# Kernel optimization log

Measured on AMD Instinct MI355X. Metric: run time of the kernel, lower is better.

## Reference

```python
import jax, jax.numpy as jnp
import numpy as np

P_TOKENS = 200  # num_prompt_tokens
N_HEADS = 4


def setup_inputs() -> dict:
    key = jax.random.key(0)
    ks = jax.random.split(key, 6)
    B, N, C = 64, 1224, 1024
    D = 256  # bottleneck / down_size
    s = 0.02
    return {
        "x": jax.random.normal(ks[0], (B, N, C), dtype=jnp.float32),
        "down_W": jax.random.normal(ks[1], (D, C), dtype=jnp.float32) * s,
        "down_b": jnp.zeros((D,), jnp.float32),
        "up_W": jax.random.normal(ks[2], (C, D), dtype=jnp.float32) * s,
        "up_b": jnp.zeros((C,), jnp.float32),
        "in_proj_W": jax.random.normal(ks[3], (3 * D, D), dtype=jnp.float32) * s,
        "in_proj_b": jnp.zeros((3 * D,), jnp.float32),
        "out_proj_W": jax.random.normal(ks[4], (D, D), dtype=jnp.float32) * s,
        "out_proj_b": jnp.zeros((D,), jnp.float32),
        "gate": jnp.float32(1.0),
    }


def _forward(x, down_W, down_b, up_W, up_b, in_proj_W, in_proj_b,
             out_proj_W, out_proj_b, gate):
    B, N, C = x.shape
    E = down_W.shape[0]
    hd = E // N_HEADS
    # down projection + exact GELU (torch nn.GELU default)
    down = jax.nn.gelu(x @ down_W.T + down_b, approximate=False)  # [B,N,E]
    prompt = down[:, :P_TOKENS, :]   # [B,P,E]
    tok = down[:, P_TOKENS:, :]      # [B,T,E]
    # --- nn.MultiheadAttention(prompt, prompt, prompt) ---
    qkv = prompt @ in_proj_W.T + in_proj_b            # [B,P,3E]
    q, k, v = jnp.split(qkv, 3, axis=-1)
    def heads(t):
        return t.reshape(B, P_TOKENS, N_HEADS, hd)
    q, k, v = heads(q), heads(k), heads(v)
    attn = jnp.einsum('bqhd,bkhd->bhqk', q, k) / jnp.sqrt(jnp.float32(hd))
    attn = jax.nn.softmax(attn, axis=-1)
    sa = jnp.einsum('bhqk,bkhd->bqhd', attn, v).reshape(B, P_TOKENS, E)
    sa = sa @ out_proj_W.T + out_proj_b               # [B,P,E]
    # --- manual cross attention prompt -> tokens ---
    scale = jnp.float32(E) ** -0.5
    cross = jax.nn.softmax(jnp.einsum('bpe,bte->bpt', sa, tok) * scale, axis=-1)
    prompt_out = jnp.einsum('bpt,bte->bpe', cross, tok)  # [B,P,E]
    combined = jnp.concatenate([prompt_out, tok], axis=1)  # [B,N,E]
    up = combined @ up_W.T + up_b                          # [B,N,C]
    return gate * up


def reference(x, down_W, down_b, up_W, up_b, in_proj_W, in_proj_b,
              out_proj_W, out_proj_b, gate):
    return _forward(x, down_W, down_b, up_W, up_b, in_proj_W, in_proj_b,
                    out_proj_W, out_proj_b, gate)
```

## Files before the change

### kernel.cpp

```cpp
#include <hip/hip_runtime.h>
#include <math.h>

#define BB 64
#define NN 1224
#define CC 1024
#define DD 256
#define PP 200
#define TT 1024
#define HH 4
#define HDD 64

typedef __attribute__((ext_vector_type(8))) short bf16x8;
typedef __attribute__((ext_vector_type(4))) float f32x4;
typedef unsigned short u16;
typedef unsigned long long u64;

__device__ __forceinline__ u16 f2bf(float f) {
  union { float f; unsigned int u; } v; v.f = f;
  unsigned int r = v.u + 0x7FFF + ((v.u >> 16) & 1);
  return (u16)(r >> 16);
}
__device__ __forceinline__ float bf2f(u16 h) {
  union { unsigned int u; float f; } v; v.u = ((unsigned int)h) << 16;
  return v.f;
}
__device__ __forceinline__ unsigned int pk2(float a, float b) {
  return (unsigned int)f2bf(a) | ((unsigned int)f2bf(b) << 16);
}
__device__ __forceinline__ void gload16(const void* g, void* l) {
  __builtin_amdgcn_global_load_lds(
      (const __attribute__((address_space(1))) void*)g,
      (__attribute__((address_space(3))) void*)l, 16, 0, 0);
}
__device__ __forceinline__ f32x4 ntld4(const float* p) {
  return __builtin_nontemporal_load((const f32x4*)p);
}

static const size_t SZ_DOWN = (size_t)BB * NN * DD * 2;
static const size_t SZ_TOKT = (size_t)BB * DD * TT * 2;
static const size_t SZ_Q    = (size_t)BB * HH * PP * HDD * 2;
static const size_t SZ_SCORES = (size_t)BB * PP * TT * 2;

static const size_t B_DOWN   = 0;
static const size_t B_TOKT   = B_DOWN + SZ_DOWN;
static const size_t B_POOL   = B_TOKT + SZ_TOKT;
static const size_t B_QB     = B_POOL;
static const size_t B_KB     = B_QB + SZ_Q;
static const size_t B_VB     = B_KB + SZ_Q;
static const size_t B_SA     = B_VB + SZ_Q;
static const size_t B_SA2    = B_SA + SZ_Q;
static const size_t B_POUTBF = B_SA2;
static const size_t B_SCORES = B_SA2 + SZ_Q;
static const size_t B_PBF    = B_SCORES;
static const size_t B_W      = B_SCORES + SZ_SCORES * 2;
static const size_t B_WD     = B_W;
static const size_t B_WU     = B_WD + 524288;
static const size_t B_WIP    = B_WU + 524288;
static const size_t B_WOP    = B_WIP + 393216;

#define MFMA_STEP64(Ab, Bb) \
  _Pragma("unroll") \
  for (int kk = 0; kk < 64; kk += 32) { \
    bf16x8 af[4], bfr[2]; \
    _Pragma("unroll") \
    for (int mi = 0; mi < 4; ++mi) { \
      const int R = mi * 16 + (lane & 15); \
      const int byt = (R * 128 + (kk + (lane >> 4) * 8) * 2) ^ ((R & 7) << 4); \
      af[mi] = *(const bf16x8*)((const char*)Ab + byt); \
    } \
    _Pragma("unroll") \
    for (int ni = 0; ni < 2; ++ni) { \
      const int R = wave * 32 + ni * 16 + (lane & 15); \
      const int byt = (R * 128 + (kk + (lane >> 4) * 8) * 2) ^ ((R & 7) << 4); \
      bfr[ni] = *(const bf16x8*)((const char*)Bb + byt); \
    } \
    _Pragma("unroll") \
    for (int mi = 0; mi < 4; ++mi) \
      _Pragma("unroll") \
      for (int ni = 0; ni < 2; ++ni) \
        acc[mi][ni] = __builtin_amdgcn_mfma_f32_16x16x32_bf16(af[mi], bfr[ni], acc[mi][ni], 0, 0, 0); \
  }

#define MFMA_AF(SACC, K0, Bbuf) \
  _Pragma("unroll") \
  for (int kk = 0; kk < 64; kk += 32) { \
    bf16x8 af[4], bfr[2]; \
    _Pragma("unroll") \
    for (int mi = 0; mi < 4; ++mi) { \
      const int R = mi * 16 + (lane & 15); \
      const int byt = (R * 512 + ((K0) + kk + (lane >> 4) * 8) * 2) ^ ((R & 7) << 4); \
      af[mi] = *(const bf16x8*)((const char*)Afull + byt); \
    } \
    _Pragma("unroll") \
    for (int ni = 0; ni < 2; ++ni) { \
      const int R = wave * 32 + ni * 16 + (lane & 15); \
      const int byt = (R * 128 + (kk + (lane >> 4) * 8) * 2) ^ ((R & 7) << 4); \
      bfr[ni] = *(const bf16x8*)((const char*)Bbuf + byt); \
    } \
    _Pragma("unroll") \
    for (int mi = 0; mi < 4; ++mi) \
      _Pragma("unroll") \
      for (int ni = 0; ni < 2; ++ni) \
        SACC[mi][ni] = __builtin_amdgcn_mfma_f32_16x16x32_bf16(af[mi], bfr[ni], SACC[mi][ni], 0, 0, 0); \
  }

#define GLOAD_A1(Ab, SRC) \
  { \
    const int L = wave * 1024 + lane * 16; \
    const int r = L >> 7; \
    const int ce = ((L & 127) ^ ((r & 7) << 4)) >> 1; \
    gload16((SRC), (char*)Ab + wave * 1024); \
  }

#define GLOAD_B4(Bb, SRC) \
  _Pragma("unroll") \
  for (int ii = 0; ii < 4; ++ii) { \
    const int slot = wave * 4 + ii; \
    const int L = slot * 1024 + lane * 16; \
    const int r = L >> 7; \
    const int ce = ((L & 127) ^ ((r & 7) << 4)) >> 1; \
    gload16((SRC), (char*)Bb + slot * 1024); \
  }

#define PIPE_WAIT(N) asm volatile("s_waitcnt vmcnt(" #N ")" ::: "memory");
#define PIPE_BAR() \
  __builtin_amdgcn_s_barrier(); \
  __builtin_amdgcn_sched_barrier(0);
#define PIPE_END() \
  asm volatile("s_waitcnt lgkmcnt(0)" ::: "memory"); \
  __builtin_amdgcn_s_barrier(); \
  __builtin_amdgcn_sched_barrier(0);

__global__ __launch_bounds__(256) void k_castw(const float* __restrict__ dW,
                                               const float* __restrict__ uW,
                                               const float* __restrict__ iW,
                                               const float* __restrict__ oW,
                                               u16* __restrict__ dWb, u16* __restrict__ uWb,
                                               u16* __restrict__ iWb, u16* __restrict__ oWb)
{
  const int id = blockIdx.x * 256 + threadIdx.x;
  const float* s; u16* d; int off;
  if (id < 65536)       { s = dW; d = dWb; off = id; }
  else if (id < 131072) { s = uW; d = uWb; off = id - 65536; }
  else if (id < 180224) { s = iW; d = iWb; off = id - 131072; }
  else                  { s = oW; d = oWb; off = id - 180224; }
  const float4 v = ((const float4*)s)[off];
  uint2 p; p.x = pk2(v.x, v.y); p.y = pk2(v.z, v.w);
  *(uint2*)&d[(size_t)off * 4] = p;
}

__global__ __launch_bounds__(512) void k_down(const float* __restrict__ x,
                                              const u16* __restrict__ Wd,
                                              const float* __restrict__ bias,
                                              u16* __restrict__ out,
                                              u16* __restrict__ tokT)
{
  __shared__ u16 Ab[2][64 * 64];
  __shared__ u16 Bb[2][256 * 64];
  const int tid = threadIdx.x;
  const int lane = tid & 63, wave = tid >> 6;
  f32x4 acc[4][2] = {};
  const int m0 = blockIdx.x * 64;
  const int ar0 = tid >> 4;
  const int c4 = (tid & 15) * 4;

  f32x4 areg[2];
#pragma unroll
  for (int i = 0; i < 2; ++i)
    areg[i] = ntld4(&x[(size_t)(m0 + ar0 + 32 * i) * CC + c4]);
#pragma unroll
  for (int i = 0; i < 2; ++i) {
    const int r = ar0 + 32 * i;
    uint2 p; p.x = pk2(areg[i].x, areg[i].y); p.y = pk2(areg[i].z, areg[i].w);
    *(uint2*)((char*)Ab[0] + ((r * 128 + c4 * 2) ^ ((r & 7) << 4))) = p;
  }
  GLOAD_B4(Bb[0], &Wd[(size_t)r * CC + 0 + ce])
#pragma unroll
  for (int i = 0; i < 2; ++i)
    areg[i] = ntld4(&x[(size_t)(m0 + ar0 + 32 * i) * CC + 64 + c4]);

  for (int it = 0; it < 16; ++it) {
    const int cur = it & 1;
    if (it < 14) {
#pragma unroll
      for (int i = 0; i < 2; ++i) {
        const int r = ar0 + 32 * i;
        uint2 p; p.x = pk2(areg[i].x, areg[i].y); p.y = pk2(areg[i].z, areg[i].w);
        *(uint2*)((char*)Ab[cur ^ 1] + ((r * 128 + c4 * 2) ^ ((r & 7) << 4))) = p;
      }
      const int kx = (it + 2) * 64;
#pragma unroll
      for (int i = 0; i < 2; ++i)
        areg[i] = ntld4(&x[(size_t)(m0 + ar0 + 32 * i) * CC + kx + c4]);
      const int kb = (it + 1) * 64;
      GLOAD_B4(Bb[cur ^ 1], &Wd[(size_t)r * CC + kb + ce])
      asm volatile("s_waitcnt vmcnt(6) lgkmcnt(0)" ::: "memory");
    } else if (it == 14) {
#pragma unroll
      for (int i = 0; i < 2; ++i) {
        const int r = ar0 + 32 * i;
        uint2 p; p.x = pk2(areg[i].x, areg[i].y); p.y = pk2(areg[i].z, areg[i].w);
        *(uint2*)((char*)Ab[cur ^ 1] + ((r * 128 + c4 * 2) ^ ((r & 7) << 4))) = p;
      }
      GLOAD_B4(Bb[cur ^ 1], &Wd[(size_t)r * CC + 960 + ce])
      asm volatile("s_waitcnt vmcnt(4) lgkmcnt(0)" ::: "memory");
    } else {
      asm volatile("s_waitcnt vmcnt(0) lgkmcnt(0)" ::: "memory");
    }
    PIPE_BAR()
    MFMA_STEP64(Ab[cur], Bb[cur])
    PIPE_END()
  }
#pragma unroll
  for (int mi = 0; mi < 4; ++mi) {
#pragma unroll
    for (int ni = 0; ni < 2; ++ni) {
      const int col = wave * 32 + ni * 16 + (lane & 15);
      const float bv = bias[col];
      u16 vs[4];
#pragma unroll
      for (int r = 0; r < 4; ++r) {
        const int row = m0 + mi * 16 + (lane >> 4) * 4 + r;
        float v = acc[mi][ni][r] + bv;
        v = 0.5f * v * (1.f + erff(v * 0.7071067811865475f));
        vs[r] = f2bf(v);
        out[(size_t)row * DD + col] = vs[r];
      }
      const int row0 = m0 + mi * 16 + (lane >> 4) * 4;
      const int b = row0 / NN, rr = row0 - b * NN;
      if (rr >= PP) {
        const u64 pk = (u64)vs[0] | ((u64)vs[1] << 16) | ((u64)vs[2] << 32) | ((u64)vs[3] << 48);
        *(u64*)&tokT[((size_t)(b * DD + col)) * TT + (rr - PP)] = pk;
      }
    }
  }
}

__global__ __launch_bounds__(512) void k_qkv(const u16* __restrict__ down,
                                             const u16* __restrict__ Wip,
                                             const float* __restrict__ bias,
                                             u16* __restrict__ qb,
                                             u16* __restrict__ kb,
                                             u16* __restrict__ vb)
{
  __shared__ u16 Ab[2][64 * 64];
  __shared__ u16 Bb[2][256 * 64];
  const int tid = threadIdx.x;
  const int lane = tid & 63, wave = tid >> 6;
  f32x4 acc[4][2] = {};
  const int m0 = blockIdx.x * 64;
  const int nt = blockIdx.y;

#define QKV_A(BUF, K0) GLOAD_A1(BUF, ({ const int m = m0 + r; const int b = m / PP; const int p = m - b * PP; \
                    &down[((size_t)(b * NN + p)) * DD + (K0) + ce]; }))
  QKV_A(Ab[0], 0)
  GLOAD_B4(Bb[0], &Wip[(size_t)(nt * 256 + r) * DD + 0 + ce])
  for (int it = 0; it < 4; ++it) {
    const int cur = it & 1;
    if (it < 3) {
      const int k0 = (it + 1) * 64;
      QKV_A(Ab[cur ^ 1], k0)
      GLOAD_B4(Bb[cur ^ 1], &Wip[(size_t)(nt * 256 + r) * DD + k0 + ce])
      PIPE_WAIT(5)
    } else { PIPE_WAIT(0) }
    PIPE_BAR()
    MFMA_STEP64(Ab[cur], Bb[cur])
    PIPE_END()
  }
#undef QKV_A
  u16* dst = (nt == 0) ? qb : ((nt == 1) ? kb : vb);
#pragma unroll
  for (int mi = 0; mi < 4; ++mi) {
#pragma unroll
    for (int ni = 0; ni < 2; ++ni) {
      const int n = wave * 32 + ni * 16 + (lane & 15);
      const float bv = bias[nt * 256 + n];
      const int h = n >> 6, dd = n & 63;
#pragma unroll
      for (int r = 0; r < 4; ++r) {
        const int m = m0 + mi * 16 + (lane >> 4) * 4 + r;
        const int b = m / PP, p = m - b * PP;
        dst[(((size_t)(b * HH + h)) * PP + p) * HDD + dd] = f2bf(acc[mi][ni][r] + bv);
      }
    }
  }
}

__global__ __launch_bounds__(512) void k_attn(const u16* __restrict__ qb,
                                              const u16* __restrict__ kb,
                                              const u16* __restrict__ vb,
                                              u16* __restrict__ sa)
{
  __shared__ u16 Ks[208 * 64];
  __shared__ u16 Vt[64 * 232];
  __shared__ u16 Pb[8 * 16 * 232];
  const int tid = threadIdx.x, lane = tid & 63, wave = tid >> 6;
  const int bh = blockIdx.x;
  const size_t kvbase = (size_t)bh * (PP * HDD);

  for (int it = 0; it < 7; ++it) {
    const int idx = tid + 512 * it;
    if (idx < 3200) {
      const int e = idx * 4;
      const int j = e >> 6, d = e & 63;
      const u64 kv = *(const u64*)&kb[kvbase + e];
      const int byt = (j * 128 + d * 2) ^ ((j & 7) << 4);
      *(u64*)((char*)Ks + byt) = kv;
      const u64 vv = *(const u64*)&vb[kvbase + e];
      const u16* vp = (const u16*)&vv;
#pragma unroll
      for (int w = 0; w < 4; ++w) Vt[(d + w) * 232 + j] = vp[w];
    }
  }
  if (tid < 128) {
    const int rr = 200 + (tid >> 4), c = (tid & 15) * 4;
    const int byt = (rr * 128 + c * 2) ^ ((rr & 7) << 4);
    *(u64*)((char*)Ks + byt) = 0ULL;
  }
  {
    const int d = tid >> 3, cg = tid & 7;
    *(u64*)&Vt[d * 232 + 200 + cg * 4] = 0ULL;
  }
  {
    u16* pw = Pb + wave * (16 * 232);
#pragma unroll
    for (int w = 0; w < 2; ++w) {
      const int idx = lane + 64 * w;
      if (idx < 96) {
        const int row = idx / 6, cg = idx - row * 6;
        *(u64*)&pw[row * 232 + 208 + cg * 4] = 0ULL;
      }
    }
  }
  __syncthreads();

  const int b_ = bh >> 2, h = bh & 3;
  const u16* qbase = qb + kvbase;
  u16* pw = Pb + wave * (16 * 232);

  for (int f = wave; f < 13; f += 8) {
    int qrow = f * 16 + (lane & 15); if (qrow > 199) qrow = 199;
    bf16x8 qa[2];
#pragma unroll
    for (int kk = 0; kk < 2; ++kk)
      qa[kk] = *(const bf16x8*)&qbase[(size_t)qrow * 64 + kk * 32 + (lane >> 4) * 8];

    f32x4 s[13];
#pragma unroll
    for (int nf = 0; nf < 13; ++nf) {
      const int R = nf * 16 + (lane & 15);
      f32x4 a = {};
#pragma unroll
      for (int kk = 0; kk < 2; ++kk) {
        const int byt = (R * 128 + (kk * 32 + (lane >> 4) * 8) * 2) ^ ((R & 7) << 4);
        const bf16x8 kf = *(const bf16x8*)((const char*)Ks + byt);
        a = __builtin_amdgcn_mfma_f32_16x16x32_bf16(qa[kk], kf, a, 0, 0, 0);
      }
      s[nf] = a;
    }
    float mx[4] = {-1e30f, -1e30f, -1e30f, -1e30f};
#pragma unroll
    for (int nf = 0; nf < 13; ++nf) {
      const int col = nf * 16 + (lane & 15);
#pragma unroll
      for (int r = 0; r < 4; ++r) {
        float v = (col < PP) ? s[nf][r] * 0.125f : -INFINITY;
        s[nf][r] = v;
        mx[r] = fmaxf(mx[r], v);
      }
    }
#pragma unroll
    for (int off = 1; off < 16; off <<= 1)
#pragma unroll
      for (int r = 0; r < 4; ++r) mx[r] = fmaxf(mx[r], __shfl_xor(mx[r], off));
    float sum[4] = {0.f, 0.f, 0.f, 0.f};
#pragma unroll
    for (int nf = 0; nf < 13; ++nf)
#pragma unroll
      for (int r = 0; r < 4; ++r) {
        const float e = expf(s[nf][r] - mx[r]);
        s[nf][r] = e;
        sum[r] += e;
      }
#pragma unroll
    for (int off = 1; off < 16; off <<= 1)
#pragma unroll
      for (int r = 0; r < 4; ++r) sum[r] += __shfl_xor(sum[r], off);
    float inv[4];
#pragma unroll
    for (int r = 0; r < 4; ++r) inv[r] = 1.f / sum[r];
#pragma unroll
    for (int nf = 0; nf < 13; ++nf) {
      const int col = nf * 16 + (lane & 15);
#pragma unroll
      for (int r = 0; r < 4; ++r) {
        const int row = (lane >> 4) * 4 + r;
        pw[row * 232 + col] = f2bf(s[nf][r] * inv[r]);
      }
    }
    f32x4 o[4] = {};
#pragma unroll
    for (int kk = 0; kk < 7; ++kk) {
      const bf16x8 pa = *(const bf16x8*)((const char*)pw +
                         ((lane & 15) * 232 + kk * 32 + (lane >> 4) * 8) * 2);
#pragma unroll
      for (int nf4 = 0; nf4 < 4; ++nf4) {
        const bf16x8 vv = *(const bf16x8*)((const char*)Vt +
                           (((lane & 15) + 16 * nf4) * 232 + kk * 32 + (lane >> 4) * 8) * 2);
        o[nf4] = __builtin_amdgcn_mfma_f32_16x16x32_bf16(pa, vv, o[nf4], 0, 0, 0);
      }
    }
#pragma unroll
    for (int nf4 = 0; nf4 < 4; ++nf4) {
      const int d = (lane & 15) + 16 * nf4;
#pragma unroll
      for (int r = 0; r < 4; ++r) {
        const int p = f * 16 + (lane >> 4) * 4 + r;
        if (p < PP)
          sa[((size_t)(b_ * PP + p)) * DD + h * HDD + d] = f2bf(o[nf4][r]);
      }
    }
  }
}

__global__ __launch_bounds__(512, 2) void k_fuse(const u16* __restrict__ A,
                                                 const u16* __restrict__ Wop,
                                                 const float* __restrict__ bias,
                                                 const u16* __restrict__ down,
                                                 u16* __restrict__ pbf)
{
  __shared__ u16 Ab[2][64 * 64];
  __shared__ u16 Bb[2][256 * 64];
  __shared__ u16 Afull[64 * 256];
  __shared__ float Mred[8][64];
  __shared__ float Lred[8][64];
  const int tid = threadIdx.x;
  const int lane = tid & 63, wave = tid >> 6;
  const int b = blockIdx.x, mh = blockIdx.y;
  const int m0 = mh * 64;

  f32x4 acc[4][2] = {};
#define FU_A(BUF, K0) GLOAD_A1(BUF, ({ int p = m0 + r; p = (p < PP) ? p : (PP - 1); \
                    &A[((size_t)(b * PP + p)) * DD + (K0) + ce]; }))
  FU_A(Ab[0], 0)
  GLOAD_B4(Bb[0], &Wop[(size_t)r * DD + 0 + ce])
  for (int it = 0; it < 4; ++it) {
    const int cur = it & 1;
    if (it < 3) {
      const int k0 = (it + 1) * 64;
      FU_A(Ab[cur ^ 1], k0)
      GLOAD_B4(Bb[cur ^ 1], &Wop[(size_t)r * DD + k0 + ce])
      PIPE_WAIT(5)
    } else { PIPE_WAIT(0) }
    PIPE_BAR()
    MFMA_STEP64(Ab[cur], Bb[cur])
    PIPE_END()
  }
#undef FU_A

  GLOAD_B4(Bb[0], &down[((size_t)(b * NN + PP + r)) * DD + 0 + ce])

#pragma unroll
  for (int mi = 0; mi < 4; ++mi) {
#pragma unroll
    for (int ni = 0; ni < 2; ++ni) {
      const int col = wave * 32 + ni * 16 + (lane & 15);
      const float bv = bias[col];
#pragma unroll
      for (int r = 0; r < 4; ++r) {
        const int row = mi * 16 + (lane >> 4) * 4 + r;
        *(u16*)((char*)Afull + ((row * 512 + col * 2) ^ ((row & 7) << 4))) =
            f2bf(acc[mi][ni][r] + bv);
      }
    }
  }
  __syncthreads();

  f32x4 s4[4][4][2] = {};
#pragma unroll
  for (int st = 0; st < 16; ++st) {
    const int cur = st & 1;
    if (st < 15) {
      const int nx = st + 1;
      const int nt2 = nx >> 2, k02 = (nx & 3) * 64;
      GLOAD_B4(Bb[cur ^ 1], &down[((size_t)(b * NN + PP + nt2 * 256 + r)) * DD + k02 + ce])
      PIPE_WAIT(4)
    } else { PIPE_WAIT(0) }
    PIPE_BAR()
    {
      const int k0s = (st & 3) * 64;
      MFMA_AF(s4[st >> 2], k0s, Bb[cur])
    }
    PIPE_END()
  }

  float mx[4][4];
#pragma unroll
  for (int mi = 0; mi < 4; ++mi)
#pragma unroll
    for (int r = 0; r < 4; ++r) mx[mi][r] = -1e30f;
#pragma unroll
  for (int nt = 0; nt < 4; ++nt)
#pragma unroll
    for (int mi = 0; mi < 4; ++mi)
#pragma unroll
      for (int ni = 0; ni < 2; ++ni)
#pragma unroll
        for (int r = 0; r < 4; ++r) {
          const float v = s4[nt][mi][ni][r] * 0.0625f;
          s4[nt][mi][ni][r] = v;
          mx[mi][r] = fmaxf(mx[mi][r], v);
        }
#pragma unroll
  for (int off = 1; off < 16; off <<= 1)
#pragma unroll
    for (int mi = 0; mi < 4; ++mi)
#pragma unroll
      for (int r = 0; r < 4; ++r) mx[mi][r] = fmaxf(mx[mi][r], __shfl_xor(mx[mi][r], off));
  if ((lane & 15) == 0) {
#pragma unroll
    for (int mi = 0; mi < 4; ++mi)
#pragma unroll
      for (int r = 0; r < 4; ++r)
        Mred[wave][mi * 16 + (lane >> 4) * 4 + r] = mx[mi][r];
  }
  __syncthreads();
  float M[4][4];
#pragma unroll
  for (int mi = 0; mi < 4; ++mi)
#pragma unroll
    for (int r = 0; r < 4; ++r) {
      const int row = mi * 16 + (lane >> 4) * 4 + r;
      float m = Mred[0][row];
#pragma unroll
      for (int w = 1; w < 8; ++w) m = fmaxf(m, Mred[w][row]);
      M[mi][r] = m;
    }
  float l[4][4];
#pragma unroll
  for (int mi = 0; mi < 4; ++mi)
#pragma unroll
    for (int r = 0; r < 4; ++r) l[mi][r] = 0.f;
#pragma unroll
  for (int nt = 0; nt < 4; ++nt)
#pragma unroll
    for (int mi = 0; mi < 4; ++mi)
#pragma unroll
      for (int ni = 0; ni < 2; ++ni)
#pragma unroll
        for (int r = 0; r < 4; ++r) {
          const float e = __expf(s4[nt][mi][ni][r] - M[mi][r]);
          s4[nt][mi][ni][r] = e;
          l[mi][r] += e;
        }
#pragma unroll
  for (int off = 1; off < 16; off <<= 1)
#pragma unroll
    for (int mi = 0; mi < 4; ++mi)
#pragma unroll
      for (int r = 0; r < 4; ++r) l[mi][r] += __shfl_xor(l[mi][r], off);
  if ((lane & 15) == 0) {
#pragma unroll
    for (int mi = 0; mi < 4; ++mi)
#pragma unroll
      for (int r = 0; r < 4; ++r)
        Lred[wave][mi * 16 + (lane >> 4) * 4 + r] = l[mi][r];
  }
  __syncthreads();
  float inv[4][4];
#pragma unroll
  for (int mi = 0; mi < 4; ++mi)
#pragma unroll
    for (int r = 0; r < 4; ++r) {
      const int row = mi * 16 + (lane >> 4) * 4 + r;
      float t = 0.f;
#pragma unroll
      for (int w = 0; w < 8; ++w) t += Lred[w][row];
      inv[mi][r] = 1.f / t;
    }

#pragma unroll
  for (int nt = 0; nt < 4; ++nt)
#pragma unroll
    for (int mi = 0; mi < 4; ++mi)
#pragma unroll
      for (int ni = 0; ni < 2; ++ni) {
        const int t = nt * 256 + wave * 32 + ni * 16 + (lane & 15);
#pragma unroll
        for (int r = 0; r < 4; ++r) {
          const int p = m0 + mi * 16 + (lane >> 4) * 4 + r;
          if (p < PP)
            pbf[((size_t)(b * PP + p)) * TT + t] = f2bf(s4[nt][mi][ni][r] * inv[mi][r]);
        }
      }
}

__global__ __launch_bounds__(512) void k_pout(const u16* __restrict__ pbf,
                                              const u16* __restrict__ tokT,
                                              u16* __restrict__ out)
{
  __shared__ u16 Ab[2][64 * 64];
  __shared__ u16 Bb[2][256 * 64];
  const int tid = threadIdx.x;
  const int lane = tid & 63, wave = tid >> 6;
  f32x4 acc[4][2] = {};
  const int b = blockIdx.x, mh = blockIdx.y;

#define PO_A(BUF, K0) GLOAD_A1(BUF, ({ int p = mh * 64 + r; p = (p < PP) ? p : (PP - 1); \
                    &pbf[((size_t)(b * PP + p)) * TT + (K0) + ce]; }))
  PO_A(Ab[0], 0)
  GLOAD_B4(Bb[0], &tokT[((size_t)(b * DD + r)) * TT + 0 + ce])
  for (int it = 0; it < 16; ++it) {
    const int cur = it & 1;
    if (it < 15) {
      const int k0 = (it + 1) * 64;
      PO_A(Ab[cur ^ 1], k0)
      GLOAD_B4(Bb[cur ^ 1], &tokT[((size_t)(b * DD + r)) * TT + k0 + ce])
      PIPE_WAIT(5)
    } else { PIPE_WAIT(0) }
    PIPE_BAR()
    MFMA_STEP64(Ab[cur], Bb[cur])
    PIPE_END()
  }
#undef PO_A
#pragma unroll
  for (int mi = 0; mi < 4; ++mi) {
#pragma unroll
    for (int ni = 0; ni < 2; ++ni) {
      const int e = wave * 32 + ni * 16 + (lane & 15);
#pragma unroll
      for (int r = 0; r < 4; ++r) {
        const int p = mh * 64 + mi * 16 + (lane >> 4) * 4 + r;
        if (p < PP)
          out[((size_t)(b * PP + p)) * DD + e] = f2bf(acc[mi][ni][r]);
      }
    }
  }
}

__global__ __launch_bounds__(512) void k_up(const u16* __restrict__ poutbf,
                                            const u16* __restrict__ down,
                                            const u16* __restrict__ Wu,
                                            const float* __restrict__ bias,
                                            const float* __restrict__ gate,
                                            float* __restrict__ out)
{
  __shared__ u16 Ab[2][64 * 64];
  __shared__ u16 Bb[2][256 * 64];
  const int tid = threadIdx.x;
  const int lane = tid & 63, wave = tid >> 6;
  f32x4 acc[4][2] = {};
  const int m0 = blockIdx.x * 64;
  const int n0 = blockIdx.y * 256;

#define UP_A(BUF, K0) GLOAD_A1(BUF, ({ const int m = m0 + r; const int b = m / NN; const int rr = m - b * NN; \
                     const u16* base = (rr < PP) ? &poutbf[((size_t)(b * PP + rr)) * DD] \
                                                 : &down[((size_t)(b * NN + rr)) * DD]; \
                     base + (K0) + ce; }))
  UP_A(Ab[0], 0)
  GLOAD_B4(Bb[0], &Wu[(size_t)(n0 + r) * DD + 0 + ce])
  for (int it = 0; it < 4; ++it) {
    const int cur = it & 1;
    if (it < 3) {
      const int k0 = (it + 1) * 64;
      UP_A(Ab[cur ^ 1], k0)
      GLOAD_B4(Bb[cur ^ 1], &Wu[(size_t)(n0 + r) * DD + k0 + ce])
      PIPE_WAIT(5)
    } else { PIPE_WAIT(0) }
    PIPE_BAR()
    MFMA_STEP64(Ab[cur], Bb[cur])
    PIPE_END()
  }
#undef UP_A
  const float g = gate[0];
#pragma unroll
  for (int mi = 0; mi < 4; ++mi) {
#pragma unroll
    for (int ni = 0; ni < 2; ++ni) {
      const int col = n0 + wave * 32 + ni * 16 + (lane & 15);
      const float bv = bias[col];
#pragma unroll
      for (int r = 0; r < 4; ++r) {
        const int row = m0 + mi * 16 + (lane >> 4) * 4 + r;
        __builtin_nontemporal_store((acc[mi][ni][r] + bv) * g, &out[(size_t)row * CC + col]);
      }
    }
  }
}

extern "C" void kernel_launch(void* const* d_in, const int* in_sizes, int n_in,
                              void* d_out, int out_size, void* d_ws, size_t ws_size,
                              hipStream_t stream) {
  const float* x          = (const float*)d_in[0];
  const float* down_W     = (const float*)d_in[1];
  const float* down_b     = (const float*)d_in[2];
  const float* up_W       = (const float*)d_in[3];
  const float* up_b       = (const float*)d_in[4];
  const float* in_proj_W  = (const float*)d_in[5];
  const float* in_proj_b  = (const float*)d_in[6];
  const float* out_proj_W = (const float*)d_in[7];
  const float* out_proj_b = (const float*)d_in[8];
  const float* gate       = (const float*)d_in[9];
  float* out = (float*)d_out;

  char* wsb = (char*)d_ws;
  u16* down_bf = (u16*)(wsb + B_DOWN);
  u16* tokT    = (u16*)(wsb + B_TOKT);
  u16* qb      = (u16*)(wsb + B_QB);
  u16* kb      = (u16*)(wsb + B_KB);
  u16* vb      = (u16*)(wsb + B_VB);
  u16* sa_bf   = (u16*)(wsb + B_SA);
  u16* pbf     = (u16*)(wsb + B_PBF);
  u16* poutbf  = (u16*)(wsb + B_POUTBF);
  u16* Wd  = (u16*)(wsb + B_WD);
  u16* Wu  = (u16*)(wsb + B_WU);
  u16* Wip = (u16*)(wsb + B_WIP);
  u16* Wop = (u16*)(wsb + B_WOP);

  k_castw<<<dim3(768), 256, 0, stream>>>(down_W, up_W, in_proj_W, out_proj_W, Wd, Wu, Wip, Wop);
  k_down<<<dim3((BB * NN) / 64), 512, 0, stream>>>(x, Wd, down_b, down_bf, tokT);
  k_qkv<<<dim3(200, 3), 512, 0, stream>>>(down_bf, Wip, in_proj_b, qb, kb, vb);
  k_attn<<<dim3(BB * HH), 512, 0, stream>>>(qb, kb, vb, sa_bf);
  k_fuse<<<dim3(BB, 4), 512, 0, stream>>>(sa_bf, Wop, out_proj_b, down_bf, pbf);
  k_pout<<<dim3(BB, 4), 512, 0, stream>>>(pbf, tokT, poutbf);
  k_up<<<dim3((BB * NN) / 64, CC / 256), 512, 0, stream>>>(poutbf, down_bf, Wu, up_b, gate, out);
}
```

Measured before the change: 306.0 us.

## Fuse cross-attention P·V into k_fuse, dropping the pbf round trip

The cross-attention probability matrix no longer goes to global memory for a separate k_pout kernel. It is written unnormalized to shared memory in two halves and multiplied against tokT inside k_fuse, with the softmax normalization applied at the end. This removes a kernel launch and the write and read of a 64x200x1024 bf16 buffer. In exchange, shared memory grows to a 128KB pool, occupancy drops to one block per CU, and the per-block serial work gets longer with only 256 blocks.

```diff
diff --git a/kernel.cpp b/kernel.cpp
--- a/kernel.cpp
+++ b/kernel.cpp
@@ -51,7 +51,6 @@
 static const size_t B_SA2    = B_SA + SZ_Q;
 static const size_t B_POUTBF = B_SA2;
 static const size_t B_SCORES = B_SA2 + SZ_Q;
-static const size_t B_PBF    = B_SCORES;
 static const size_t B_W      = B_SCORES + SZ_SCORES * 2;
 static const size_t B_WD     = B_W;
 static const size_t B_WU     = B_WD + 524288;
@@ -66,13 +65,13 @@
     for (int mi = 0; mi < 4; ++mi) { \
       const int R = mi * 16 + (lane & 15); \
       const int byt = (R * 128 + (kk + (lane >> 4) * 8) * 2) ^ ((R & 7) << 4); \
-      af[mi] = *(const bf16x8*)((const char*)Ab + byt); \
+      af[mi] = *(const bf16x8*)((const char*)(Ab) + byt); \
     } \
     _Pragma("unroll") \
     for (int ni = 0; ni < 2; ++ni) { \
       const int R = wave * 32 + ni * 16 + (lane & 15); \
       const int byt = (R * 128 + (kk + (lane >> 4) * 8) * 2) ^ ((R & 7) << 4); \
-      bfr[ni] = *(const bf16x8*)((const char*)Bb + byt); \
+      bfr[ni] = *(const bf16x8*)((const char*)(Bb) + byt); \
     } \
     _Pragma("unroll") \
     for (int mi = 0; mi < 4; ++mi) \
@@ -95,13 +94,36 @@
     for (int ni = 0; ni < 2; ++ni) { \
       const int R = wave * 32 + ni * 16 + (lane & 15); \
       const int byt = (R * 128 + (kk + (lane >> 4) * 8) * 2) ^ ((R & 7) << 4); \
-      bfr[ni] = *(const bf16x8*)((const char*)Bbuf + byt); \
+      bfr[ni] = *(const bf16x8*)((const char*)(Bbuf) + byt); \
     } \
     _Pragma("unroll") \
     for (int mi = 0; mi < 4; ++mi) \
       _Pragma("unroll") \
       for (int ni = 0; ni < 2; ++ni) \
         SACC[mi][ni] = __builtin_amdgcn_mfma_f32_16x16x32_bf16(af[mi], bfr[ni], SACC[mi][ni], 0, 0, 0); \
+  }
+
+#define MFMA_PV(O, T0, Bbuf) \
+  _Pragma("unroll") \
+  for (int kk = 0; kk < 64; kk += 32) { \
+    bf16x8 af[4], bfr[2]; \
+    _Pragma("unroll") \
+    for (int mi = 0; mi < 4; ++mi) { \
+      const int R = mi * 16 + (lane & 15); \
+      const int byt = (R * 1024 + ((T0) + kk + (lane >> 4) * 8) * 2) ^ ((R & 7) << 4); \
+      af[mi] = *(const bf16x8*)((const char*)Ph + byt); \
+    } \
+    _Pragma("unroll") \
+    for (int ni = 0; ni < 2; ++ni) { \
+      const int R = wave * 32 + ni * 16 + (lane & 15); \
+      const int byt = (R * 128 + (kk + (lane >> 4) * 8) * 2) ^ ((R & 7) << 4); \
+      bfr[ni] = *(const bf16x8*)((const char*)(Bbuf) + byt); \
+    } \
+    _Pragma("unroll") \
+    for (int mi = 0; mi < 4; ++mi) \
+      _Pragma("unroll") \
+      for (int ni = 0; ni < 2; ++ni) \
+        O[mi][ni] = __builtin_amdgcn_mfma_f32_16x16x32_bf16(af[mi], bfr[ni], O[mi][ni], 0, 0, 0); \
   }
 
 #define GLOAD_A1(Ab, SRC) \
@@ -109,7 +131,7 @@
     const int L = wave * 1024 + lane * 16; \
     const int r = L >> 7; \
     const int ce = ((L & 127) ^ ((r & 7) << 4)) >> 1; \
-    gload16((SRC), (char*)Ab + wave * 1024); \
+    gload16((SRC), (char*)(Ab) + wave * 1024); \
   }
 
 #define GLOAD_B4(Bb, SRC) \
@@ -119,7 +141,7 @@
     const int L = slot * 1024 + lane * 16; \
     const int r = L >> 7; \
     const int ce = ((L & 127) ^ ((r & 7) << 4)) >> 1; \
-    gload16((SRC), (char*)Bb + slot * 1024); \
+    gload16((SRC), (char*)(Bb) + slot * 1024); \
   }
 
 #define PIPE_WAIT(N) asm volatile("s_waitcnt vmcnt(" #N ")" ::: "memory");
@@ -127,6 +149,10 @@
   __builtin_amdgcn_s_barrier(); \
   __builtin_amdgcn_sched_barrier(0);
 #define PIPE_END() \
+  asm volatile("s_waitcnt lgkmcnt(0)" ::: "memory"); \
+  __builtin_amdgcn_s_barrier(); \
+  __builtin_amdgcn_sched_barrier(0);
+#define LGKM_BAR() \
   asm volatile("s_waitcnt lgkmcnt(0)" ::: "memory"); \
   __builtin_amdgcn_s_barrier(); \
   __builtin_amdgcn_sched_barrier(0);
@@ -423,17 +449,22 @@
   }
 }
 
-__global__ __launch_bounds__(512, 2) void k_fuse(const u16* __restrict__ A,
+__global__ __launch_bounds__(512, 1) void k_fuse(const u16* __restrict__ A,
                                                  const u16* __restrict__ Wop,
                                                  const float* __restrict__ bias,
                                                  const u16* __restrict__ down,
-                                                 u16* __restrict__ pbf)
+                                                 const u16* __restrict__ tokT,
+                                                 u16* __restrict__ pout)
 {
-  __shared__ u16 Ab[2][64 * 64];
-  __shared__ u16 Bb[2][256 * 64];
-  __shared__ u16 Afull[64 * 256];
+  __shared__ __align__(16) char pool[131072];
   __shared__ float Mred[8][64];
   __shared__ float Lred[8][64];
+  u16* Bb0 = (u16*)pool;
+  u16* Bb1 = (u16*)(pool + 32768);
+  u16* Ab0 = (u16*)(pool + 65536);
+  u16* Ab1 = (u16*)(pool + 65536 + 8192);
+  u16* Afull = (u16*)(pool + 65536);
+  u16* Ph = (u16*)(pool + 65536);
   const int tid = threadIdx.x;
   const int lane = tid & 63, wave = tid >> 6;
   const int b = blockIdx.x, mh = blockIdx.y;
@@ -442,23 +473,26 @@
   f32x4 acc[4][2] = {};
 #define FU_A(BUF, K0) GLOAD_A1(BUF, ({ int p = m0 + r; p = (p < PP) ? p : (PP - 1); \
                     &A[((size_t)(b * PP + p)) * DD + (K0) + ce]; }))
-  FU_A(Ab[0], 0)
-  GLOAD_B4(Bb[0], &Wop[(size_t)r * DD + 0 + ce])
+  FU_A(Ab0, 0)
+  GLOAD_B4(Bb0, &Wop[(size_t)r * DD + 0 + ce])
   for (int it = 0; it < 4; ++it) {
-    const int cur = it & 1;
+    u16* Abc = (it & 1) ? Ab1 : Ab0;
+    u16* Bbc = (it & 1) ? Bb1 : Bb0;
+    u16* Abn = (it & 1) ? Ab0 : Ab1;
+    u16* Bbn = (it & 1) ? Bb0 : Bb1;
     if (it < 3) {
       const int k0 = (it + 1) * 64;
-      FU_A(Ab[cur ^ 1], k0)
-      GLOAD_B4(Bb[cur ^ 1], &Wop[(size_t)r * DD + k0 + ce])
+      FU_A(Abn, k0)
+      GLOAD_B4(Bbn, &Wop[(size_t)r * DD + k0 + ce])
       PIPE_WAIT(5)
     } else { PIPE_WAIT(0) }
     PIPE_BAR()
-    MFMA_STEP64(Ab[cur], Bb[cur])
+    MFMA_STEP64(Abc, Bbc)
     PIPE_END()
   }
 #undef FU_A
 
-  GLOAD_B4(Bb[0], &down[((size_t)(b * NN + PP + r)) * DD + 0 + ce])
+  GLOAD_B4(Bb0, &down[((size_t)(b * NN + PP + r)) * DD + 0 + ce])
 
 #pragma unroll
   for (int mi = 0; mi < 4; ++mi) {
@@ -474,25 +508,28 @@
       }
     }
   }
-  __syncthreads();
+  LGKM_BAR()
 
   f32x4 s4[4][4][2] = {};
 #pragma unroll
   for (int st = 0; st < 16; ++st) {
-    const int cur = st & 1;
+    u16* Bbc = (st & 1) ? Bb1 : Bb0;
+    u16* Bbn = (st & 1) ? Bb0 : Bb1;
     if (st < 15) {
       const int nx = st + 1;
       const int nt2 = nx >> 2, k02 = (nx & 3) * 64;
-      GLOAD_B4(Bb[cur ^ 1], &down[((size_t)(b * NN + PP + nt2 * 256 + r)) * DD + k02 + ce])
+      GLOAD_B4(Bbn, &down[((size_t)(b * NN + PP + nt2 * 256 + r)) * DD + k02 + ce])
       PIPE_WAIT(4)
     } else { PIPE_WAIT(0) }
     PIPE_BAR()
     {
       const int k0s = (st & 3) * 64;
-      MFMA_AF(s4[st >> 2], k0s, Bb[cur])
+      MFMA_AF(s4[st >> 2], k0s, Bbc)
     }
     PIPE_END()
   }
+
+  GLOAD_B4(Bb0, &tokT[((size_t)(b * DD + r)) * TT + 0 + ce])
 
   float mx[4][4];
 #pragma unroll
@@ -524,7 +561,7 @@
       for (int r = 0; r < 4; ++r)
         Mred[wave][mi * 16 + (lane >> 4) * 4 + r] = mx[mi][r];
   }
-  __syncthreads();
+  LGKM_BAR()
   float M[4][4];
 #pragma unroll
   for (int mi = 0; mi < 4; ++mi)
@@ -566,7 +603,7 @@
       for (int r = 0; r < 4; ++r)
         Lred[wave][mi * 16 + (lane >> 4) * 4 + r] = l[mi][r];
   }
-  __syncthreads();
+  LGKM_BAR()
   float inv[4][4];
 #pragma unroll
   for (int mi = 0; mi < 4; ++mi)
@@ -579,50 +616,56 @@
       inv[mi][r] = 1.f / t;
     }
 
-#pragma unroll
-  for (int nt = 0; nt < 4; ++nt)
-#pragma unroll
-    for (int mi = 0; mi < 4; ++mi)
-#pragma unroll
-      for (int ni = 0; ni < 2; ++ni) {
-        const int t = nt * 256 + wave * 32 + ni * 16 + (lane & 15);
-#pragma unroll
-        for (int r = 0; r < 4; ++r) {
-          const int p = m0 + mi * 16 + (lane >> 4) * 4 + r;
-          if (p < PP)
-            pbf[((size_t)(b * PP + p)) * TT + t] = f2bf(s4[nt][mi][ni][r] * inv[mi][r]);
-        }
-      }
-}
-
-__global__ __launch_bounds__(512) void k_pout(const u16* __restrict__ pbf,
-                                              const u16* __restrict__ tokT,
-                                              u16* __restrict__ out)
-{
-  __shared__ u16 Ab[2][64 * 64];
-  __shared__ u16 Bb[2][256 * 64];
-  const int tid = threadIdx.x;
-  const int lane = tid & 63, wave = tid >> 6;
-  f32x4 acc[4][2] = {};
-  const int b = blockIdx.x, mh = blockIdx.y;
-
-#define PO_A(BUF, K0) GLOAD_A1(BUF, ({ int p = mh * 64 + r; p = (p < PP) ? p : (PP - 1); \
-                    &pbf[((size_t)(b * PP + p)) * TT + (K0) + ce]; }))
-  PO_A(Ab[0], 0)
-  GLOAD_B4(Bb[0], &tokT[((size_t)(b * DD + r)) * TT + 0 + ce])
-  for (int it = 0; it < 16; ++it) {
-    const int cur = it & 1;
-    if (it < 15) {
-      const int k0 = (it + 1) * 64;
-      PO_A(Ab[cur ^ 1], k0)
-      GLOAD_B4(Bb[cur ^ 1], &tokT[((size_t)(b * DD + r)) * TT + k0 + ce])
-      PIPE_WAIT(5)
+  f32x4 o[4][2] = {};
+#define WRITE_P(NT0) \
+  _Pragma("unroll") \
+  for (int q = 0; q < 2; ++q) \
+    _Pragma("unroll") \
+    for (int mi = 0; mi < 4; ++mi) \
+      _Pragma("unroll") \
+      for (int ni = 0; ni < 2; ++ni) { \
+        const int tl = q * 256 + wave * 32 + ni * 16 + (lane & 15); \
+        _Pragma("unroll") \
+        for (int r = 0; r < 4; ++r) { \
+          const int row = mi * 16 + (lane >> 4) * 4 + r; \
+          *(u16*)((char*)Ph + ((row * 1024 + tl * 2) ^ ((row & 7) << 4))) = \
+              f2bf(s4[(NT0) + q][mi][ni][r]); \
+        } \
+      }
+
+  WRITE_P(0)
+  LGKM_BAR()
+#pragma unroll
+  for (int st = 0; st < 8; ++st) {
+    u16* Bbc = (st & 1) ? Bb1 : Bb0;
+    u16* Bbn = (st & 1) ? Bb0 : Bb1;
+    if (st < 7) {
+      GLOAD_B4(Bbn, &tokT[((size_t)(b * DD + r)) * TT + (st + 1) * 64 + ce])
+      PIPE_WAIT(4)
+    } else {
+      GLOAD_B4(Bbn, &tokT[((size_t)(b * DD + r)) * TT + 512 + ce])
+      PIPE_WAIT(4)
+    }
+    PIPE_BAR()
+    MFMA_PV(o, st * 64, Bbc)
+    PIPE_END()
+  }
+  WRITE_P(2)
+  LGKM_BAR()
+#pragma unroll
+  for (int st = 0; st < 8; ++st) {
+    u16* Bbc = (st & 1) ? Bb1 : Bb0;
+    u16* Bbn = (st & 1) ? Bb0 : Bb1;
+    if (st < 7) {
+      GLOAD_B4(Bbn, &tokT[((size_t)(b * DD + r)) * TT + 512 + (st + 1) * 64 + ce])
+      PIPE_WAIT(4)
     } else { PIPE_WAIT(0) }
     PIPE_BAR()
-    MFMA_STEP64(Ab[cur], Bb[cur])
+    MFMA_PV(o, st * 64, Bbc)
     PIPE_END()
   }
-#undef PO_A
+#undef WRITE_P
+
 #pragma unroll
   for (int mi = 0; mi < 4; ++mi) {
 #pragma unroll
@@ -630,9 +673,9 @@
       const int e = wave * 32 + ni * 16 + (lane & 15);
 #pragma unroll
       for (int r = 0; r < 4; ++r) {
-        const int p = mh * 64 + mi * 16 + (lane >> 4) * 4 + r;
+        const int p = m0 + mi * 16 + (lane >> 4) * 4 + r;
         if (p < PP)
-          out[((size_t)(b * PP + p)) * DD + e] = f2bf(acc[mi][ni][r]);
+          pout[((size_t)(b * PP + p)) * DD + e] = f2bf(o[mi][ni][r] * inv[mi][r]);
       }
     }
   }
@@ -710,7 +753,6 @@
   u16* kb      = (u16*)(wsb + B_KB);
   u16* vb      = (u16*)(wsb + B_VB);
   u16* sa_bf   = (u16*)(wsb + B_SA);
-  u16* pbf     = (u16*)(wsb + B_PBF);
   u16* poutbf  = (u16*)(wsb + B_POUTBF);
   u16* Wd  = (u16*)(wsb + B_WD);
   u16* Wu  = (u16*)(wsb + B_WU);
@@ -721,7 +763,6 @@
   k_down<<<dim3((BB * NN) / 64), 512, 0, stream>>>(x, Wd, down_b, down_bf, tokT);
   k_qkv<<<dim3(200, 3), 512, 0, stream>>>(down_bf, Wip, in_proj_b, qb, kb, vb);
   k_attn<<<dim3(BB * HH), 512, 0, stream>>>(qb, kb, vb, sa_bf);
-  k_fuse<<<dim3(BB, 4), 512, 0, stream>>>(sa_bf, Wop, out_proj_b, down_bf, pbf);
-  k_pout<<<dim3(BB, 4), 512, 0, stream>>>(pbf, tokT, poutbf);
+  k_fuse<<<dim3(BB, 4), 512, 0, stream>>>(sa_bf, Wop, out_proj_b, down_bf, tokT, poutbf);
   k_up<<<dim3((BB * NN) / 64, CC / 256), 512, 0, stream>>>(poutbf, down_bf, Wu, up_b, gate, out);
 }
```

Measured after the change: 318.3 us. +4.0%, slower.
